# Optimization experiments

Hardware: AMD Instinct MI355X
Metric: run time of the kernel (lower is better)

The kernel has to match this reference:

```python
import jax, jax.numpy as jnp
import numpy as np

SEQ, D_IN, D_OUT = 8192, 1024, 1024

def setup_inputs() -> dict:
    key = jax.random.key(0)
    kx, kq, kk, kv = jax.random.split(key, 4)
    x = jax.random.normal(kx, (SEQ, D_IN), dtype=jnp.float32)
    # original uses torch.rand (uniform [0,1)) for parameters
    W_query = jax.random.uniform(kq, (D_IN, D_OUT), dtype=jnp.float32)
    W_key = jax.random.uniform(kk, (D_IN, D_OUT), dtype=jnp.float32)
    W_value = jax.random.uniform(kv, (D_IN, D_OUT), dtype=jnp.float32)
    return {"x": x, "W_query": W_query, "W_key": W_key, "W_value": W_value}

def reference(x, W_query, W_key, W_value):
    # x: [S, d_in]; projections: [S, d_out]
    queries = x @ W_query
    keys = x @ W_key
    values = x @ W_value
    scale = 1.0 / jnp.sqrt(jnp.asarray(keys.shape[-1], dtype=x.dtype))
    attn_scores = jnp.einsum('sd,td->st', queries, keys) * scale  # [S, S]
    attn_weights = jax.nn.softmax(attn_scores, axis=-1)
    context_vec = attn_weights @ values  # [S, d_out]
    return context_vec
```

## Files before the change

kernel.cpp:

```cpp
#include <hip/hip_runtime.h>
#include <hip/hip_bf16.h>
#include <hip/hip_fp16.h>

#define SEQ 8192
#define DM  1024

typedef __attribute__((ext_vector_type(8))) short    bf16x8;
typedef __attribute__((ext_vector_type(8))) _Float16 f16x8;
typedef __attribute__((ext_vector_type(4))) float    f32x4;

union H8 { _Float16 h[8]; int4 v; };

__device__ __forceinline__ unsigned short f2bf(float f) {
    union { float f; unsigned u; } x; x.f = f;
    unsigned r = x.u + 0x7fffu + ((x.u >> 16) & 1u);
    return (unsigned short)(r >> 16);
}
__device__ __forceinline__ float bf2f(unsigned short h) {
    union { unsigned u; float f; } x; x.u = ((unsigned)h) << 16;
    return x.f;
}

__device__ __forceinline__ void gld16(const unsigned short* g, unsigned short* l) {
    __builtin_amdgcn_global_load_lds(
        (const __attribute__((address_space(1))) void*)g,
        (__attribute__((address_space(3))) void*)l, 16, 0, 0);
}

__global__ __launch_bounds__(256) void prep_kernel(const float* __restrict__ x,
    unsigned short* __restrict__ xhi, unsigned short* __restrict__ xlo,
    const float* W0, const float* W1, const float* W2,
    unsigned short* H0, unsigned short* L0,
    unsigned short* H1, unsigned short* L1,
    unsigned short* H2, unsigned short* L2)
{
    __shared__ float tile[64][65];
    int t = threadIdx.x;

    if (blockIdx.x < 8192) {
        int base = (blockIdx.x * 256 + t) * 4;
        float4 v = *(const float4*)(x + base);
        float f[4] = {v.x, v.y, v.z, v.w};
        unsigned short h[4], l[4];
#pragma unroll
        for (int j = 0; j < 4; j++) { h[j] = f2bf(f[j]); l[j] = f2bf(f[j] - bf2f(h[j])); }
        ushort4 hv = {h[0], h[1], h[2], h[3]};
        ushort4 lv = {l[0], l[1], l[2], l[3]};
        *(ushort4*)(xhi + base) = hv;
        *(ushort4*)(xlo + base) = lv;
        return;
    }

    int id = blockIdx.x - 8192;
    int z  = id >> 8;
    int rem = id & 255;
    int bn = (rem & 15) * 64;
    int bk = (rem >> 4) * 64;
    const float* W = (z == 0) ? W0 : (z == 1) ? W1 : W2;
    unsigned short* Wthi = (z == 0) ? H0 : (z == 1) ? H1 : H2;
    unsigned short* Wtlo = (z == 0) ? L0 : (z == 1) ? L1 : L2;

#pragma unroll
    for (int p = 0; p < 4; p++) {
        int r = p * 16 + (t >> 4);
        int c = (t & 15) * 4;
        float4 v = *(const float4*)(W + (size_t)(bk + r) * DM + bn + c);
        tile[r][c] = v.x; tile[r][c+1] = v.y; tile[r][c+2] = v.z; tile[r][c+3] = v.w;
    }
    __syncthreads();
#pragma unroll
    for (int p = 0; p < 2; p++) {
        int task = p * 256 + t;
        int rn = task >> 3;
        int kc = (task & 7) * 8;
        union { unsigned short u[8]; int4 v; } hh, ll;
#pragma unroll
        for (int j = 0; j < 8; j++) {
            float f = tile[kc + j][rn];
            hh.u[j] = f2bf(f);
            ll.u[j] = f2bf(f - bf2f(hh.u[j]));
        }
        size_t o = (size_t)(bn + rn) * DM + bk + kc;
        *(int4*)(Wthi + o) = hh.v;
        *(int4*)(Wtlo + o) = ll.v;
    }
}

template<int MODE, int KD>
__global__ __launch_bounds__(256) void gemm128(
    const unsigned short* A,   const unsigned short* Alo,
    const unsigned short* B_,  const unsigned short* Blo_,
    const unsigned short* B2,  const unsigned short* B2lo,
    unsigned short* Chi_, unsigned short* Clo_,
    unsigned short* Chi2, unsigned short* Clo2,
    _Float16* Cf16, float* Cf32, const float* __restrict__ Scp)
{
    constexpr bool SPLIT = (MODE == 0);
    __shared__ alignas(16) unsigned short sAhi[128 * 32];
    __shared__ alignas(16) unsigned short sBhi[128 * 32];
    __shared__ alignas(16) unsigned short sAlo[SPLIT ? 128 * 32 : 16];
    __shared__ alignas(16) unsigned short sBlo[SPLIT ? 128 * 32 : 16];
    __shared__ alignas(16) _Float16 sSc[(MODE == 3) ? 128 * 130 : 8];

    const unsigned short* B   = B_;
    const unsigned short* Blo = Blo_;
    unsigned short* Chi = Chi_;
    unsigned short* Clo = Clo_;
    if (MODE == 0 && blockIdx.z == 1) { B = B2; Blo = B2lo; Chi = Chi2; Clo = Clo2; }

    const int m0 = blockIdx.x * 128;
    const int n0 = blockIdx.y * 128;
    const int t = threadIdx.x;
    const int wave = t >> 6, lane = t & 63;
    const int wr = wave >> 1, wc = wave & 1;
    const int i16 = lane & 15, quad = lane >> 4;

    const int rs = wave * 32 + (lane >> 2);
    const int cs = (lane & 3) * 8;
    const size_t aoff = (size_t)(m0 + rs) * KD + cs;
    const size_t boff = (size_t)(n0 + rs) * KD + cs;
    const int ldsb = wave * 1024;

    if constexpr (MODE == 3) {
#pragma unroll
        for (int i = 0; i < 16; i++) {
            int idx = i * 1024 + t * 4;
            int row = idx >> 7, col = idx & 127;
            float4 v = *(const float4*)(Scp + (size_t)(m0 + row) * 128 + col);
            _Float16* d = sSc + row * 130 + col;
            d[0] = (_Float16)v.x; d[1] = (_Float16)v.y;
            d[2] = (_Float16)v.z; d[3] = (_Float16)v.w;
        }
    }

    f32x4 acc[4][4] = {};

    for (int k = 0; k < KD; k += 32) {
        __syncthreads();
        gld16(A + aoff + k,            sAhi + ldsb);
        gld16(A + aoff + 16 * KD + k,  sAhi + ldsb + 512);
        gld16(B + boff + k,            sBhi + ldsb);
        gld16(B + boff + 16 * KD + k,  sBhi + ldsb + 512);
        if constexpr (SPLIT) {
            gld16(Alo + aoff + k,           sAlo + ldsb);
            gld16(Alo + aoff + 16 * KD + k, sAlo + ldsb + 512);
            gld16(Blo + boff + k,           sBlo + ldsb);
            gld16(Blo + boff + 16 * KD + k, sBlo + ldsb + 512);
        }
        __syncthreads();

        _Float16 sch[4];
        if constexpr (MODE == 3) {
#pragma unroll
            for (int mt = 0; mt < 4; mt++)
                sch[mt] = sSc[(wr * 64 + mt * 16 + i16) * 130 + (k >> 6)];
        }

        bf16x8 ahi[4], alo[4];
#pragma unroll
        for (int mt = 0; mt < 4; mt++) {
            int r = wr * 64 + mt * 16 + i16;
            ahi[mt] = *(const bf16x8*)(sAhi + r * 32 + quad * 8);
            if constexpr (MODE == 3) {
                f16x8 av = __builtin_bit_cast(f16x8, ahi[mt]);
                av = av * sch[mt];
                ahi[mt] = __builtin_bit_cast(bf16x8, av);
            }
            if constexpr (SPLIT) alo[mt] = *(const bf16x8*)(sAlo + r * 32 + quad * 8);
        }
#pragma unroll
        for (int nt = 0; nt < 4; nt++) {
            int r = wc * 64 + nt * 16 + i16;
            bf16x8 bhi = *(const bf16x8*)(sBhi + r * 32 + quad * 8);
            bf16x8 blo;
            if constexpr (SPLIT) blo = *(const bf16x8*)(sBlo + r * 32 + quad * 8);
#pragma unroll
            for (int mt = 0; mt < 4; mt++) {
                if constexpr (MODE == 3) {
                    acc[mt][nt] = __builtin_amdgcn_mfma_f32_16x16x32_f16(
                        __builtin_bit_cast(f16x8, ahi[mt]), __builtin_bit_cast(f16x8, bhi),
                        acc[mt][nt], 0, 0, 0);
                } else {
                    acc[mt][nt] = __builtin_amdgcn_mfma_f32_16x16x32_bf16(ahi[mt], bhi, acc[mt][nt], 0, 0, 0);
                    if constexpr (SPLIT) {
                        acc[mt][nt] = __builtin_amdgcn_mfma_f32_16x16x32_bf16(ahi[mt], blo, acc[mt][nt], 0, 0, 0);
                        acc[mt][nt] = __builtin_amdgcn_mfma_f32_16x16x32_bf16(alo[mt], bhi, acc[mt][nt], 0, 0, 0);
                    }
                }
            }
        }
    }

    if constexpr (MODE == 0) {
#pragma unroll
        for (int mt = 0; mt < 4; mt++)
#pragma unroll
            for (int nt = 0; nt < 4; nt++)
#pragma unroll
                for (int r = 0; r < 4; r++) {
                    int row = m0 + wr * 64 + mt * 16 + quad * 4 + r;
                    int col = n0 + wc * 64 + nt * 16 + i16;
                    float v = acc[mt][nt][r];
                    unsigned short h = f2bf(v);
                    Chi[(size_t)row * DM + col] = h;
                    Clo[(size_t)row * DM + col] = f2bf(v - bf2f(h));
                }
    } else if constexpr (MODE == 1) {
#pragma unroll
        for (int mt = 0; mt < 4; mt++)
#pragma unroll
            for (int nt = 0; nt < 4; nt++)
#pragma unroll
                for (int r = 0; r < 4; r++) {
                    int row = m0 + wr * 64 + mt * 16 + quad * 4 + r;
                    int col = n0 + wc * 64 + nt * 16 + i16;
                    Cf16[(size_t)row * DM + col] = (_Float16)acc[mt][nt][r];
                }
    } else {
#pragma unroll
        for (int mt = 0; mt < 4; mt++)
#pragma unroll
            for (int nt = 0; nt < 4; nt++)
#pragma unroll
                for (int r = 0; r < 4; r++) {
                    int row = m0 + wr * 64 + mt * 16 + quad * 4 + r;
                    int col = n0 + wc * 64 + nt * 16 + i16;
                    Cf32[(size_t)row * DM + col] = acc[mt][nt][r];
                }
    }
}

__global__ __launch_bounds__(512, 2) void scores256(
    const unsigned short* __restrict__ Qh, const unsigned short* __restrict__ Ql,
    const unsigned short* __restrict__ Kh, const unsigned short* __restrict__ Kl,
    _Float16* __restrict__ Eo, float* __restrict__ Tt, float* __restrict__ Zt)
{
    constexpr int KD = 1024;
    constexpr int NT = KD / 32;
    __shared__ alignas(16) unsigned short lds[2 * 4 * 8192];

    const int flat = blockIdx.y * gridDim.x + blockIdx.x;
    const int wg = (flat & 7) * 128 + (flat >> 3);
    const int m0 = (wg >> 5) << 8;
    const int n0 = (wg & 31) << 8;

    const int t = threadIdx.x;
    const int wave = t >> 6, lane = t & 63;
    const int wr = wave >> 2, wc = wave & 3;
    const int i16 = lane & 15, quad = lane >> 4;

    const int srow = wave * 16 + (lane >> 2);
    const int scol = ((lane & 3) ^ ((lane >> 3) & 3)) << 3;
    const size_t ga = (size_t)(m0 + srow) * KD + scol;
    const size_t gb = (size_t)(n0 + srow) * KD + scol;
    const int ldw = wave * 512;

    int offA[8], offB[4];
#pragma unroll
    for (int mt = 0; mt < 8; mt++) {
        int row = wr * 128 + mt * 16 + i16;
        offA[mt] = row * 32 + ((quad ^ ((row >> 1) & 3)) << 3);
    }
#pragma unroll
    for (int nt = 0; nt < 4; nt++) {
        int row = wc * 64 + nt * 16 + i16;
        offB[nt] = row * 32 + ((quad ^ ((row >> 1) & 3)) << 3);
    }

    f32x4 acc[8][4] = {};

    auto STAGE = [&](int buf, int kt) {
        unsigned short* p = lds + buf * 32768;
        const int k = kt * 32;
#pragma unroll
        for (int i = 0; i < 2; i++) {
            const size_t gAo = ga + (size_t)(i * 128) * KD + k;
            const size_t gBo = gb + (size_t)(i * 128) * KD + k;
            const int lo = ldw + i * 4096;
            gld16(Qh + gAo, p + lo);
            gld16(Ql + gAo, p + 8192  + lo);
            gld16(Kh + gBo, p + 16384 + lo);
            gld16(Kl + gBo, p + 24576 + lo);
        }
    };

    STAGE(0, 0);
    asm volatile("s_waitcnt vmcnt(0)" ::: "memory");
    __builtin_amdgcn_s_barrier();
    __builtin_amdgcn_sched_barrier(0);

    for (int kt = 0; kt < NT; ++kt) {
        const int cur = kt & 1;
        const unsigned short* pAh = lds + cur * 32768;
        const unsigned short* pAl = pAh + 8192;
        const unsigned short* pBh = pAh + 16384;
        const unsigned short* pBl = pAh + 24576;

        bf16x8 ah[4], al[4], bh[4], bl[4];

#pragma unroll
        for (int mi = 0; mi < 4; mi++) {
            ah[mi] = *(const bf16x8*)(pAh + offA[mi]);
            al[mi] = *(const bf16x8*)(pAl + offA[mi]);
        }
#pragma unroll
        for (int ni = 0; ni < 4; ni++) {
            bh[ni] = *(const bf16x8*)(pBh + offB[ni]);
            bl[ni] = *(const bf16x8*)(pBl + offB[ni]);
        }
        if (kt + 1 < NT) STAGE(cur ^ 1, kt + 1);

        __builtin_amdgcn_s_setprio(1);
#pragma unroll
        for (int mi = 0; mi < 4; mi++)
#pragma unroll
            for (int ni = 0; ni < 4; ni++) {
                f32x4 c = acc[mi][ni];
                c = __builtin_amdgcn_mfma_f32_16x16x32_bf16(ah[mi], bh[ni], c, 0, 0, 0);
                c = __builtin_amdgcn_mfma_f32_16x16x32_bf16(ah[mi], bl[ni], c, 0, 0, 0);
                c = __builtin_amdgcn_mfma_f32_16x16x32_bf16(al[mi], bh[ni], c, 0, 0, 0);
                acc[mi][ni] = c;
            }
        __builtin_amdgcn_s_setprio(0);

#pragma unroll
        for (int mi = 0; mi < 4; mi++) {
            ah[mi] = *(const bf16x8*)(pAh + offA[4 + mi]);
            al[mi] = *(const bf16x8*)(pAl + offA[4 + mi]);
        }

        __builtin_amdgcn_s_setprio(1);
#pragma unroll
        for (int mi = 0; mi < 4; mi++)
#pragma unroll
            for (int ni = 0; ni < 4; ni++) {
                f32x4 c = acc[4 + mi][ni];
                c = __builtin_amdgcn_mfma_f32_16x16x32_bf16(ah[mi], bh[ni], c, 0, 0, 0);
                c = __builtin_amdgcn_mfma_f32_16x16x32_bf16(ah[mi], bl[ni], c, 0, 0, 0);
                c = __builtin_amdgcn_mfma_f32_16x16x32_bf16(al[mi], bh[ni], c, 0, 0, 0);
                acc[4 + mi][ni] = c;
            }
        __builtin_amdgcn_s_setprio(0);

        asm volatile("s_waitcnt vmcnt(0)" ::: "memory");
        __builtin_amdgcn_s_barrier();
        __builtin_amdgcn_sched_barrier(0);
    }

    const float scale = 0.03125f;
    const int tix = (n0 + wc * 64) >> 6;
#pragma unroll
    for (int mt = 0; mt < 8; mt++)
#pragma unroll
        for (int r = 0; r < 4; r++) {
            float s0 = acc[mt][0][r] * scale, s1 = acc[mt][1][r] * scale;
            float s2 = acc[mt][2][r] * scale, s3 = acc[mt][3][r] * scale;
            float mx = fmaxf(fmaxf(s0, s1), fmaxf(s2, s3));
            mx = fmaxf(mx, __shfl_xor(mx, 1));
            mx = fmaxf(mx, __shfl_xor(mx, 2));
            mx = fmaxf(mx, __shfl_xor(mx, 4));
            mx = fmaxf(mx, __shfl_xor(mx, 8));
            float e0 = __expf(s0 - mx), e1 = __expf(s1 - mx);
            float e2 = __expf(s2 - mx), e3 = __expf(s3 - mx);
            float z = e0 + e1 + e2 + e3;
            z += __shfl_xor(z, 1);
            z += __shfl_xor(z, 2);
            z += __shfl_xor(z, 4);
            z += __shfl_xor(z, 8);
            int row = m0 + wr * 128 + mt * 16 + quad * 4 + r;
            if (i16 == 0) {
                Tt[(size_t)row * 128 + tix] = mx;
                Zt[(size_t)row * 128 + tix] = z;
            }
            size_t eb = (size_t)row * SEQ + n0 + wc * 64 + i16;
            Eo[eb +  0] = (_Float16)e0;
            Eo[eb + 16] = (_Float16)e1;
            Eo[eb + 32] = (_Float16)e2;
            Eo[eb + 48] = (_Float16)e3;
        }
}

__global__ __launch_bounds__(256) void transpose_f16(const _Float16* __restrict__ in,
                                                     _Float16* __restrict__ out)
{
    __shared__ _Float16 tile[64][72];
    int bn = blockIdx.x * 64;
    int bm = blockIdx.y * 64;
    int t = threadIdx.x;
    int r = t >> 3, c = (t & 7) * 8;
#pragma unroll
    for (int p = 0; p < 2; p++) {
        int rr = p * 32 + r;
        H8 v; v.v = *(const int4*)(in + (size_t)(bm + rr) * DM + bn + c);
#pragma unroll
        for (int j = 0; j < 8; j++) tile[rr][c + j] = v.h[j];
    }
    __syncthreads();
#pragma unroll
    for (int p = 0; p < 2; p++) {
        int rr = p * 32 + r;
        H8 v;
#pragma unroll
        for (int j = 0; j < 8; j++) v.h[j] = tile[c + j][rr];
        *(int4*)(out + (size_t)(bn + rr) * SEQ + bm + c) = v.v;
    }
}

__global__ __launch_bounds__(256) void sc_reduce(const float* __restrict__ Tt,
    const float* __restrict__ Zt, float* __restrict__ Sc)
{
    int row = blockIdx.x * 4 + (threadIdx.x >> 6);
    int lane = threadIdx.x & 63;
    size_t b = (size_t)row * 128 + lane;
    float t0 = Tt[b], t1 = Tt[b + 64];
    float z0 = Zt[b], z1 = Zt[b + 64];
    float m = fmaxf(t0, t1);
    for (int sh = 1; sh < 64; sh <<= 1) m = fmaxf(m, __shfl_xor(m, sh));
    float l = z0 * __expf(t0 - m) + z1 * __expf(t1 - m);
    for (int sh = 1; sh < 64; sh <<= 1) l += __shfl_xor(l, sh);
    float inv = 1.0f / l;
    Sc[b]      = __expf(t0 - m) * inv;
    Sc[b + 64] = __expf(t1 - m) * inv;
}

extern "C" void kernel_launch(void* const* d_in, const int* in_sizes, int n_in,
                              void* d_out, int out_size, void* d_ws, size_t ws_size,
                              hipStream_t stream)
{
    const float* x  = (const float*)d_in[0];
    const float* Wq = (const float*)d_in[1];
    const float* Wk = (const float*)d_in[2];
    const float* Wv = (const float*)d_in[3];
    float* Out = (float*)d_out;
    char* ws = (char*)d_ws;

    const size_t MB = 1024 * 1024;
    unsigned short* xhi   = (unsigned short*)(ws + 0 * MB);
    unsigned short* xlo   = (unsigned short*)(ws + 16 * MB);
    unsigned short* Wqthi = (unsigned short*)(ws + 32 * MB);
    unsigned short* Wqtlo = (unsigned short*)(ws + 34 * MB);
    unsigned short* Wkthi = (unsigned short*)(ws + 36 * MB);
    unsigned short* Wktlo = (unsigned short*)(ws + 38 * MB);
    unsigned short* Wvthi = (unsigned short*)(ws + 40 * MB);
    unsigned short* Wvtlo = (unsigned short*)(ws + 42 * MB);
    _Float16*       Vtmp  = (_Float16*)     (ws + 44 * MB);
    _Float16*       E     = (_Float16*)     (ws + 0 * MB);

    size_t off = 128 * MB;
    unsigned short* Qhi = (unsigned short*)(ws + off); off += 16 * MB;
    unsigned short* Qlo = (unsigned short*)(ws + off); off += 16 * MB;
    unsigned short* Khi = (unsigned short*)(ws + off); off += 16 * MB;
    unsigned short* Klo = (unsigned short*)(ws + off); off += 16 * MB;
    _Float16*       Vt  = (_Float16*)      (ws + off); off += 16 * MB;
    float*          Tt  = (float*)         (ws + off); off += (size_t)SEQ * 128 * 4;
    float*          Zt  = (float*)         (ws + off); off += (size_t)SEQ * 128 * 4;
    float*          Sc  = (float*)         (ws + off); off += (size_t)SEQ * 128 * 4;

    prep_kernel<<<8192 + 768, 256, 0, stream>>>(x, xhi, xlo, Wq, Wk, Wv,
        Wqthi, Wqtlo, Wkthi, Wktlo, Wvthi, Wvtlo);
    gemm128<0, DM><<<dim3(SEQ / 128, DM / 128, 2), 256, 0, stream>>>(
        xhi, xlo, Wqthi, Wqtlo, Wkthi, Wktlo,
        Qhi, Qlo, Khi, Klo, nullptr, nullptr, nullptr);
    gemm128<1, DM><<<dim3(SEQ / 128, DM / 128), 256, 0, stream>>>(
        xhi, nullptr, Wvthi, nullptr, nullptr, nullptr,
        nullptr, nullptr, nullptr, nullptr, (_Float16*)Vtmp, nullptr, nullptr);
    transpose_f16<<<dim3(DM / 64, SEQ / 64), 256, 0, stream>>>(Vtmp, Vt);
    scores256<<<dim3(SEQ / 256, SEQ / 256), 512, 0, stream>>>(
        Qhi, Qlo, Khi, Klo, E, Tt, Zt);
    sc_reduce<<<SEQ / 4, 256, 0, stream>>>(Tt, Zt, Sc);
    gemm128<3, SEQ><<<dim3(SEQ / 128, DM / 128), 256, 0, stream>>>(
        (const unsigned short*)E, nullptr, (const unsigned short*)Vt, nullptr, nullptr, nullptr,
        nullptr, nullptr, nullptr, nullptr, nullptr, Out, Sc);
}
```

Measured before the change: 776.5 us.

## Double-buffer LDS tiles with swizzled layout and overlap loads with MFMA

Converts the gemm128 K-loop to double-buffered shared memory. The next tile is issued via global_load_lds while MFMAs run on the current tile, and a single barrier per iteration replaces two. It also XOR-swizzles the LDS column layout to reduce bank conflicts on fragment reads, raises wave priority around the MFMA block, and adds a launch-bounds occupancy hint. The trade-off is doubled LDS use (up to 64KB in split mode), which may lower occupancy.

```diff
diff --git a/kernel.cpp b/kernel.cpp
--- a/kernel.cpp
+++ b/kernel.cpp
@@ -87,7 +87,7 @@
 }
 
 template<int MODE, int KD>
-__global__ __launch_bounds__(256) void gemm128(
+__global__ __launch_bounds__(256, 2) void gemm128(
     const unsigned short* A,   const unsigned short* Alo,
     const unsigned short* B_,  const unsigned short* Blo_,
     const unsigned short* B2,  const unsigned short* B2lo,
@@ -96,10 +96,11 @@
     _Float16* Cf16, float* Cf32, const float* __restrict__ Scp)
 {
     constexpr bool SPLIT = (MODE == 0);
-    __shared__ alignas(16) unsigned short sAhi[128 * 32];
-    __shared__ alignas(16) unsigned short sBhi[128 * 32];
-    __shared__ alignas(16) unsigned short sAlo[SPLIT ? 128 * 32 : 16];
-    __shared__ alignas(16) unsigned short sBlo[SPLIT ? 128 * 32 : 16];
+    constexpr int NT = KD / 32;
+    __shared__ alignas(16) unsigned short sAhi[2][128 * 32];
+    __shared__ alignas(16) unsigned short sBhi[2][128 * 32];
+    __shared__ alignas(16) unsigned short sAlo[SPLIT ? 2 * 128 * 32 : 16];
+    __shared__ alignas(16) unsigned short sBlo[SPLIT ? 2 * 128 * 32 : 16];
     __shared__ alignas(16) _Float16 sSc[(MODE == 3) ? 128 * 130 : 8];
 
     const unsigned short* B   = B_;
@@ -116,10 +117,22 @@
     const int i16 = lane & 15, quad = lane >> 4;
 
     const int rs = wave * 32 + (lane >> 2);
-    const int cs = (lane & 3) * 8;
-    const size_t aoff = (size_t)(m0 + rs) * KD + cs;
-    const size_t boff = (size_t)(n0 + rs) * KD + cs;
+    const int scol = ((lane & 3) ^ ((lane >> 3) & 3)) << 3;
+    const size_t aoff = (size_t)(m0 + rs) * KD + scol;
+    const size_t boff = (size_t)(n0 + rs) * KD + scol;
     const int ldsb = wave * 1024;
+
+    int offA[4], offB[4];
+#pragma unroll
+    for (int mt = 0; mt < 4; mt++) {
+        int row = wr * 64 + mt * 16 + i16;
+        offA[mt] = row * 32 + ((quad ^ ((row >> 1) & 3)) << 3);
+    }
+#pragma unroll
+    for (int nt = 0; nt < 4; nt++) {
+        int row = wc * 64 + nt * 16 + i16;
+        offB[nt] = row * 32 + ((quad ^ ((row >> 1) & 3)) << 3);
+    }
 
     if constexpr (MODE == 3) {
 #pragma unroll
@@ -133,62 +146,73 @@
         }
     }
 
+    auto STAGE = [&](int buf, int k) {
+        gld16(A + aoff + k,           sAhi[buf] + ldsb);
+        gld16(A + aoff + 16 * KD + k, sAhi[buf] + ldsb + 512);
+        gld16(B + boff + k,           sBhi[buf] + ldsb);
+        gld16(B + boff + 16 * KD + k, sBhi[buf] + ldsb + 512);
+        if constexpr (SPLIT) {
+            gld16(Alo + aoff + k,           sAlo + buf * 4096 + ldsb);
+            gld16(Alo + aoff + 16 * KD + k, sAlo + buf * 4096 + ldsb + 512);
+            gld16(Blo + boff + k,           sBlo + buf * 4096 + ldsb);
+            gld16(Blo + boff + 16 * KD + k, sBlo + buf * 4096 + ldsb + 512);
+        }
+    };
+
     f32x4 acc[4][4] = {};
 
-    for (int k = 0; k < KD; k += 32) {
-        __syncthreads();
-        gld16(A + aoff + k,            sAhi + ldsb);
-        gld16(A + aoff + 16 * KD + k,  sAhi + ldsb + 512);
-        gld16(B + boff + k,            sBhi + ldsb);
-        gld16(B + boff + 16 * KD + k,  sBhi + ldsb + 512);
-        if constexpr (SPLIT) {
-            gld16(Alo + aoff + k,           sAlo + ldsb);
-            gld16(Alo + aoff + 16 * KD + k, sAlo + ldsb + 512);
-            gld16(Blo + boff + k,           sBlo + ldsb);
-            gld16(Blo + boff + 16 * KD + k, sBlo + ldsb + 512);
-        }
-        __syncthreads();
-
-        _Float16 sch[4];
+    STAGE(0, 0);
+    __syncthreads();
+
+    for (int kt = 0; kt < NT; ++kt) {
+        const int cur = kt & 1;
+        const int k = kt * 32;
+
+        bf16x8 ahi[4], alo[4], bhi[4], blo[4];
+#pragma unroll
+        for (int mt = 0; mt < 4; mt++) {
+            ahi[mt] = *(const bf16x8*)(sAhi[cur] + offA[mt]);
+            if constexpr (SPLIT) alo[mt] = *(const bf16x8*)(sAlo + cur * 4096 + offA[mt]);
+        }
+#pragma unroll
+        for (int nt = 0; nt < 4; nt++) {
+            bhi[nt] = *(const bf16x8*)(sBhi[cur] + offB[nt]);
+            if constexpr (SPLIT) blo[nt] = *(const bf16x8*)(sBlo + cur * 4096 + offB[nt]);
+        }
         if constexpr (MODE == 3) {
 #pragma unroll
-            for (int mt = 0; mt < 4; mt++)
-                sch[mt] = sSc[(wr * 64 + mt * 16 + i16) * 130 + (k >> 6)];
-        }
-
-        bf16x8 ahi[4], alo[4];
-#pragma unroll
-        for (int mt = 0; mt < 4; mt++) {
-            int r = wr * 64 + mt * 16 + i16;
-            ahi[mt] = *(const bf16x8*)(sAhi + r * 32 + quad * 8);
-            if constexpr (MODE == 3) {
+            for (int mt = 0; mt < 4; mt++) {
+                _Float16 sc = sSc[(wr * 64 + mt * 16 + i16) * 130 + (k >> 6)];
                 f16x8 av = __builtin_bit_cast(f16x8, ahi[mt]);
-                av = av * sch[mt];
+                av = av * sc;
                 ahi[mt] = __builtin_bit_cast(bf16x8, av);
             }
-            if constexpr (SPLIT) alo[mt] = *(const bf16x8*)(sAlo + r * 32 + quad * 8);
-        }
-#pragma unroll
-        for (int nt = 0; nt < 4; nt++) {
-            int r = wc * 64 + nt * 16 + i16;
-            bf16x8 bhi = *(const bf16x8*)(sBhi + r * 32 + quad * 8);
-            bf16x8 blo;
-            if constexpr (SPLIT) blo = *(const bf16x8*)(sBlo + r * 32 + quad * 8);
+        }
+
+        if (kt + 1 < NT) STAGE(cur ^ 1, k + 32);
+
+        __builtin_amdgcn_s_setprio(1);
+#pragma unroll
+        for (int nt = 0; nt < 4; nt++)
 #pragma unroll
             for (int mt = 0; mt < 4; mt++) {
                 if constexpr (MODE == 3) {
                     acc[mt][nt] = __builtin_amdgcn_mfma_f32_16x16x32_f16(
-                        __builtin_bit_cast(f16x8, ahi[mt]), __builtin_bit_cast(f16x8, bhi),
+                        __builtin_bit_cast(f16x8, ahi[mt]), __builtin_bit_cast(f16x8, bhi[nt]),
                         acc[mt][nt], 0, 0, 0);
                 } else {
-                    acc[mt][nt] = __builtin_amdgcn_mfma_f32_16x16x32_bf16(ahi[mt], bhi, acc[mt][nt], 0, 0, 0);
+                    acc[mt][nt] = __builtin_amdgcn_mfma_f32_16x16x32_bf16(ahi[mt], bhi[nt], acc[mt][nt], 0, 0, 0);
                     if constexpr (SPLIT) {
-                        acc[mt][nt] = __builtin_amdgcn_mfma_f32_16x16x32_bf16(ahi[mt], blo, acc[mt][nt], 0, 0, 0);
-                        acc[mt][nt] = __builtin_amdgcn_mfma_f32_16x16x32_bf16(alo[mt], bhi, acc[mt][nt], 0, 0, 0);
+                        acc[mt][nt] = __builtin_amdgcn_mfma_f32_16x16x32_bf16(ahi[mt], blo[nt], acc[mt][nt], 0, 0, 0);
+                        acc[mt][nt] = __builtin_amdgcn_mfma_f32_16x16x32_bf16(alo[mt], bhi[nt], acc[mt][nt], 0, 0, 0);
                     }
                 }
             }
-        }
+        __builtin_amdgcn_s_setprio(0);
+
+        asm volatile("s_waitcnt vmcnt(0)" ::: "memory");
+        __builtin_amdgcn_s_barrier();
+        __builtin_amdgcn_sched_barrier(0);
     }
 
     if constexpr (MODE == 0) {
```

Result: faster. 709.6 us (-8.6%).
